# Optimization experiments

Measured on AMD Instinct MI355X. Metric: run time of the kernel, lower is better.

Reference implementation:

```python
import jax, jax.numpy as jnp
import numpy as np

H = 1024
EPS = 1e-5
MIX_SCALE = 0.1


def setup_inputs() -> dict:
    key = jax.random.key(0)
    ks = jax.random.split(key, 6)
    B, S = 8, 4096
    x = jax.random.normal(ks[0], (B, S, H), dtype=jnp.float32)
    # to_complex: Linear(H, 2H); store weight as [H, 2H] for x @ W
    W_to = jax.random.normal(ks[1], (H, 2 * H), dtype=jnp.float32) * (1.0 / np.sqrt(H))
    b_to = jax.random.normal(ks[2], (2 * H,), dtype=jnp.float32) * 0.01
    # from_complex: Linear(2H, H)
    W_from = jax.random.normal(ks[3], (2 * H, H), dtype=jnp.float32) * (1.0 / np.sqrt(2 * H))
    b_from = jax.random.normal(ks[4], (H,), dtype=jnp.float32) * 0.01
    phase_shifts = jnp.zeros((1, 1, H), dtype=jnp.float32)
    return {"x": x, "W_to": W_to, "b_to": b_to, "W_from": W_from,
            "b_from": b_from, "phase_shifts": phase_shifts}


def reference(x, W_to, b_to, W_from, b_from, phase_shifts):
    # x: [B,S,H]
    complex_repr = x @ W_to + b_to                      # [B,S,2H]
    real, imag = jnp.split(complex_repr, 2, axis=-1)    # each [B,S,H]
    magnitude = jnp.sqrt(real**2 + imag**2 + EPS)
    phase = jnp.arctan2(imag, real)                     # [B,S,H]
    # mean_j cos(phase_i - phase_j + shift)
    #   = cos(phase_i + shift) * mean_j cos(phase_j)
    #   + sin(phase_i + shift) * mean_j sin(phase_j)
    # (exact trig identity; replaces the [B,S,S,H] materialization)
    mean_cos = jnp.mean(jnp.cos(phase), axis=1, keepdims=True)  # [B,1,H]
    mean_sin = jnp.mean(jnp.sin(phase), axis=1, keepdims=True)  # [B,1,H]
    shifted = phase + phase_shifts                              # [B,S,H]
    mixed_phase = jnp.cos(shifted) * mean_cos + jnp.sin(shifted) * mean_sin
    new_phase = phase + mixed_phase * MIX_SCALE
    new_real = magnitude * jnp.cos(new_phase)
    new_imag = magnitude * jnp.sin(new_phase)
    new_complex = jnp.concatenate([new_real, new_imag], axis=-1)  # [B,S,2H]
    return new_complex @ W_from + b_from                          # [B,S,H]
```

## Files before the change

kernel.cpp:

```cpp
#include <hip/hip_runtime.h>
#include <hip/hip_bf16.h>
#include <math.h>

#define H 1024
#define N1 2048
#define BATCH 8
#define SEQ 4096
#define M_TOT (BATCH*SEQ)
#define EPS 1e-5f
#define MIX 0.1f

typedef __attribute__((ext_vector_type(8))) short bf16x8;
typedef __attribute__((ext_vector_type(4))) float f32x4;
typedef unsigned int uint_t;

static __device__ __forceinline__ float bf2f(unsigned short u) {
    return __uint_as_float(((unsigned)u) << 16);
}
static __device__ __forceinline__ unsigned short f2bf(float x) {
    __hip_bfloat16 h = __float2bfloat16(x);
    return *reinterpret_cast<unsigned short*>(&h);
}
static __device__ __forceinline__ void gload16(const void* g, void* l) {
    __builtin_amdgcn_global_load_lds(
        (const __attribute__((address_space(1))) unsigned int*)g,
        (__attribute__((address_space(3))) unsigned int*)l,
        16, 0, 0);
}
static __device__ __forceinline__ int perm2h(int c)  { return ((c & 1023) << 1) | (c >> 10); }

__global__ __launch_bounds__(256) void cvt_f32_bf16(
    const float* __restrict__ in, unsigned short* __restrict__ out, size_t n)
{
    size_t i = ((size_t)blockIdx.x * 256 + threadIdx.x) * 8;
    if (i >= n) return;
    float4 a = *(const float4*)(in + i);
    float4 b = *(const float4*)(in + i + 4);
    union { unsigned short u[8]; uint4 v; } p;
    p.u[0] = f2bf(a.x); p.u[1] = f2bf(a.y); p.u[2] = f2bf(a.z); p.u[3] = f2bf(a.w);
    p.u[4] = f2bf(b.x); p.u[5] = f2bf(b.y); p.u[6] = f2bf(b.z); p.u[7] = f2bf(b.w);
    *(uint4*)(out + i) = p.v;
}

__global__ __launch_bounds__(256) void transpose_wt(
    const float* __restrict__ in, unsigned short* __restrict__ out)
{
    __shared__ float tile[64][65];
    const int c0 = blockIdx.x * 64, r0 = blockIdx.y * 64;
    const int tc = threadIdx.x & 63, tr4 = (threadIdx.x >> 6) * 16;
    #pragma unroll
    for (int rr = 0; rr < 16; ++rr)
        tile[tr4 + rr][tc] = in[(size_t)(r0 + tr4 + rr) * N1 + c0 + tc];
    __syncthreads();
    #pragma unroll
    for (int rr = 0; rr < 16; ++rr)
        out[(size_t)perm2h(c0 + tr4 + rr) * H + r0 + tc] = f2bf(tile[tc][tr4 + rr]);
}

__global__ __launch_bounds__(256) void transpose_wf(
    const float* __restrict__ in, unsigned short* __restrict__ out)
{
    __shared__ float tile[64][65];
    const int n0 = blockIdx.x * 64, k0 = blockIdx.y * 64;
    const int tc = threadIdx.x & 63, tr4 = (threadIdx.x >> 6) * 16;
    #pragma unroll
    for (int rr = 0; rr < 16; ++rr) {
        const int k = k0 + tr4 + rr;
        tile[tr4 + rr][tc] = in[(size_t)((k >> 1) | ((k & 1) << 10)) * H + n0 + tc];
    }
    __syncthreads();
    #pragma unroll
    for (int rr = 0; rr < 16; ++rr)
        out[(size_t)(n0 + tr4 + rr) * N1 + k0 + tc] = f2bf(tile[tc][tr4 + rr]);
}

#define VM4 asm volatile("s_waitcnt vmcnt(4)" ::: "memory")
#define VM0 asm volatile("s_waitcnt vmcnt(0)" ::: "memory")

#define STG(X, BB, HH, CC, TT) \
    gload16(X##g + (size_t)((HH)*128 + (CC)*64) * KDIM + (TT)*64, \
            &X##s[BB][(HH)*8192 + (CC)*4096 + t*8])
#define STAGE_HT(X, BB, HH, TT) do { STG(X, BB, HH, 0, TT); STG(X, BB, HH, 1, TT); } while(0)

#define LDA(BB, MF, KS) (*(const bf16x8*)&As[BB][(wr*128 + (MF)*16 + fr)*64 + ((((KS)*4 + lg) ^ rsw))*8])
#define LDB(BB, NF, KS) (*(const bf16x8*)&Bs[BB][(wc*64  + (NF)*16 + fr)*64 + ((((KS)*4 + lg) ^ rsw))*8])

#define PHASE(BB, Q, STAGE_STMT, VM_STMT) do {                                  \
    if ((Q) == 0) {                                                             \
        _Pragma("unroll")                                                       \
        for (int nf = 0; nf < 4; ++nf) {                                        \
            bfr[nf][0] = LDB(BB, nf, 0);                                        \
            bfr[nf][1] = LDB(BB, nf, 1);                                        \
        }                                                                       \
    }                                                                           \
    afr[0][0] = LDA(BB, 2*(Q),   0); afr[0][1] = LDA(BB, 2*(Q),   1);           \
    afr[1][0] = LDA(BB, 2*(Q)+1, 0); afr[1][1] = LDA(BB, 2*(Q)+1, 1);           \
    STAGE_STMT;                                                                 \
    __builtin_amdgcn_s_barrier();                                               \
    asm volatile("s_waitcnt lgkmcnt(0)" ::: "memory");                          \
    __builtin_amdgcn_sched_barrier(0);                                          \
    __builtin_amdgcn_s_setprio(1);                                              \
    _Pragma("unroll")                                                           \
    for (int nf = 0; nf < 4; ++nf) {                                            \
        acc[2*(Q)][nf]   = __builtin_amdgcn_mfma_f32_16x16x32_bf16(afr[0][0], bfr[nf][0], acc[2*(Q)][nf],   0,0,0); \
        acc[2*(Q)][nf]   = __builtin_amdgcn_mfma_f32_16x16x32_bf16(afr[0][1], bfr[nf][1], acc[2*(Q)][nf],   0,0,0); \
        acc[2*(Q)+1][nf] = __builtin_amdgcn_mfma_f32_16x16x32_bf16(afr[1][0], bfr[nf][0], acc[2*(Q)+1][nf], 0,0,0); \
        acc[2*(Q)+1][nf] = __builtin_amdgcn_mfma_f32_16x16x32_bf16(afr[1][1], bfr[nf][1], acc[2*(Q)+1][nf], 0,0,0); \
    }                                                                           \
    __builtin_amdgcn_s_setprio(0);                                              \
    VM_STMT;                                                                    \
    __builtin_amdgcn_s_barrier();                                               \
} while (0)

template<int KDIM, bool G1>
__global__ __launch_bounds__(512, 2) void gemm8(
    const unsigned short* __restrict__ A,
    const unsigned short* __restrict__ Bt,
    const float* __restrict__ bias,
    void* __restrict__ Cout,
    float* __restrict__ sums)
{
    __shared__ __align__(16) unsigned short As[2][16384];
    __shared__ __align__(16) unsigned short Bs[2][16384];

    const int t    = threadIdx.x;
    const int lane = t & 63;
    const int wid  = t >> 6;
    const int wr   = wid >> 2;
    const int wc   = wid & 3;

    int m0, n0;
    if (G1) {
        const unsigned wg = ((blockIdx.x & 7) << 7) | (blockIdx.x >> 3);
        n0 = (wg & 7) * 256;
        m0 = (wg >> 3) * 256;
    } else {
        const unsigned wg = ((blockIdx.x & 7) << 6) | (blockIdx.x >> 3);
        n0 = (wg & 3) * 256;
        m0 = (wg >> 2) * 256;
    }

    const int srow = t >> 3;
    const int ssw  = ((srow >> 1) & 1) | (((srow >> 2) & 1) << 1);
    const int gk   = ((t & 7) ^ ssw) * 8;
    const unsigned short* Ag = A  + (size_t)(m0 + srow) * KDIM + gk;
    const unsigned short* Bg = Bt + (size_t)(n0 + srow) * KDIM + gk;

    const int fr  = lane & 15;
    const int lg  = lane >> 4;
    const int rsw = ((fr >> 1) & 1) | (((fr >> 2) & 1) << 1);

    f32x4 acc[8][4] = {};
    bf16x8 bfr[4][2];
    bf16x8 afr[2][2];

    constexpr int NITER = KDIM / 128;

    STAGE_HT(A, 0, 0, 0); STAGE_HT(A, 0, 1, 0);
    STAGE_HT(B, 0, 0, 0); STAGE_HT(B, 0, 1, 0);
    STAGE_HT(B, 1, 0, 1); STAGE_HT(B, 1, 1, 1);
    VM4;
    __builtin_amdgcn_s_barrier();

    for (int it = 0; it < NITER; ++it) {
        const int  T1   = 2 * it + 1;
        const int  T2   = 2 * it + 2;
        const int  T3   = 2 * it + 3;
        const bool more = (it + 1 < NITER);
        PHASE(0, 0, STAGE_HT(A, 1, 0, T1), );
        PHASE(0, 1, STAGE_HT(A, 1, 1, T1), );
        PHASE(0, 2, if (more) STAGE_HT(B, 0, 0, T2), );
        PHASE(0, 3, if (more) STAGE_HT(B, 0, 1, T2), if (more) { VM4; } else { VM0; });
        PHASE(1, 0, if (more) STAGE_HT(A, 0, 0, T2), );
        PHASE(1, 1, if (more) STAGE_HT(A, 0, 1, T2), );
        PHASE(1, 2, if (more) STAGE_HT(B, 1, 0, T3), );
        PHASE(1, 3, if (more) STAGE_HT(B, 1, 1, T3), if (more) { VM4; });
    }

    const int colbase = n0 + wc * 64;
    if (G1) {
        unsigned short* c1 = (unsigned short*)Cout;
        float lc[4] = {0, 0, 0, 0}, ls[4] = {0, 0, 0, 0};
        #pragma unroll
        for (int nf = 0; nf < 4; ++nf) {
            const int col = colbase + nf * 16 + fr;
            const float bb = bias[(col >> 1) | ((col & 1) << 10)];
            #pragma unroll
            for (int mf = 0; mf < 8; ++mf) {
                #pragma unroll
                for (int r = 0; r < 4; ++r) {
                    const float v = acc[mf][nf][r] + bb;
                    const size_t row = (size_t)(m0 + wr * 128 + mf * 16 + lg * 4 + r);
                    c1[row * N1 + col] = f2bf(v);
                    const float oth = __shfl_xor(v, 1);
                    const float re = (fr & 1) ? oth : v;
                    const float im = (fr & 1) ? v : oth;
                    const float rq = rsqrtf(fmaxf(re * re + im * im, 1e-30f));
                    lc[nf] += re * rq;
                    ls[nf] += im * rq;
                }
            }
        }
        #pragma unroll
        for (int nf = 0; nf < 4; ++nf) {
            lc[nf] += __shfl_xor(lc[nf], 16); lc[nf] += __shfl_xor(lc[nf], 32);
            ls[nf] += __shfl_xor(ls[nf], 16); ls[nf] += __shfl_xor(ls[nf], 32);
        }
        if (lane < 16 && !(lane & 1)) {
            const int b = m0 >> 12;
            #pragma unroll
            for (int nf = 0; nf < 4; ++nf) {
                const int hh = (colbase + nf * 16 + fr) >> 1;
                atomicAdd(&sums[(b * 2 + 0) * H + hh], lc[nf]);
                atomicAdd(&sums[(b * 2 + 1) * H + hh], ls[nf]);
            }
        }
    } else {
        float* o = (float*)Cout;
        #pragma unroll
        for (int nf = 0; nf < 4; ++nf) {
            const int col = colbase + nf * 16 + fr;
            const float bb = bias[col];
            #pragma unroll
            for (int mf = 0; mf < 8; ++mf) {
                #pragma unroll
                for (int r = 0; r < 4; ++r) {
                    const size_t row = (size_t)(m0 + wr * 128 + mf * 16 + lg * 4 + r);
                    o[row * H + col] = acc[mf][nf][r] + bb;
                }
            }
        }
    }
}

__global__ void finalize_pq(const float* __restrict__ sums, const float* __restrict__ ps,
                            float* __restrict__ P, float* __restrict__ Q)
{
    int i = blockIdx.x * 256 + threadIdx.x;
    int b = i >> 10, h = i & (H - 1);
    float mc = sums[(b * 2 + 0) * H + h] * (1.0f / SEQ);
    float ms = sums[(b * 2 + 1) * H + h] * (1.0f / SEQ);
    float cp = cosf(ps[h]), sp = sinf(ps[h]);
    P[i] = mc * cp + ms * sp;
    Q[i] = ms * cp - mc * sp;
}

__global__ __launch_bounds__(256) void phase_mix(
    unsigned short* __restrict__ c1, const float* __restrict__ P,
    const float* __restrict__ Q)
{
    const size_t total = (size_t)M_TOT * N1 / 8;
    for (size_t q = (size_t)blockIdx.x * 256 + threadIdx.x; q < total;
         q += (size_t)gridDim.x * 256) {
        const size_t m = q >> 8;
        const int off = ((int)q & 255) * 8;
        const int b = (int)(m >> 12);
        const int h0 = off >> 1;
        uint4* cu = (uint4*)c1;
        const size_t idx = ((size_t)m * N1 + off) >> 3;
        uint4 v = cu[idx];
        float4 Pv = *(const float4*)&P[b * H + h0];
        float4 Qv = *(const float4*)&Q[b * H + h0];
        const uint_t w[4] = { v.x, v.y, v.z, v.w };
        const float Pk[4] = { Pv.x, Pv.y, Pv.z, Pv.w };
        const float Qk[4] = { Qv.x, Qv.y, Qv.z, Qv.w };
        uint_t o[4];
        #pragma unroll
        for (int e = 0; e < 4; ++e) {
            float r  = bf2f(w[e] & 0xffff);
            float im = bf2f(w[e] >> 16);
            float tt = r * r + im * im;
            float minv = rsqrtf(fmaxf(tt, 1e-30f));
            float d = MIX * (r * Pk[e] + im * Qk[e]) * minv;
            float d2 = d * d;
            float cd = 1.0f - d2 * (0.5f - d2 * (1.0f / 24.0f));
            float sd = d * (1.0f - d2 * ((1.0f / 6.0f) - d2 * (1.0f / 120.0f)));
            float sc = sqrtf(tt + EPS) * minv;
            o[e] = (uint_t)f2bf(sc * (r * cd - im * sd))
                 | ((uint_t)f2bf(sc * (im * cd + r * sd)) << 16);
        }
        v.x = o[0]; v.y = o[1]; v.z = o[2]; v.w = o[3];
        cu[idx] = v;
    }
}

extern "C" void kernel_launch(void* const* d_in, const int* in_sizes, int n_in,
                              void* d_out, int out_size, void* d_ws, size_t ws_size,
                              hipStream_t stream) {
    const float* x  = (const float*)d_in[0];
    const float* Wt = (const float*)d_in[1];
    const float* bt = (const float*)d_in[2];
    const float* Wf = (const float*)d_in[3];
    const float* bf = (const float*)d_in[4];
    const float* ps = (const float*)d_in[5];
    float* out = (float*)d_out;

    const size_t c1_bytes   = (size_t)M_TOT * N1 * 2;
    const size_t wft_bytes  = (size_t)H * N1 * 2;
    const size_t sums_bytes = (size_t)BATCH * 2 * H * 4;
    const size_t pq_bytes   = (size_t)BATCH * H * 4;
    if (ws_size < c1_bytes + wft_bytes + sums_bytes + 2 * pq_bytes) return;

    unsigned short* c1  = (unsigned short*)d_ws;
    unsigned short* WfT = (unsigned short*)((char*)d_ws + c1_bytes);
    float* sums = (float*)((char*)d_ws + c1_bytes + wft_bytes);
    float* Pb   = (float*)((char*)d_ws + c1_bytes + wft_bytes + sums_bytes);
    float* Qb   = (float*)((char*)d_ws + c1_bytes + wft_bytes + sums_bytes + pq_bytes);

    unsigned short* xb  = (unsigned short*)d_out;
    unsigned short* WtT = (unsigned short*)d_out + (size_t)M_TOT * H;

    hipMemsetAsync(sums, 0, sums_bytes, stream);

    cvt_f32_bf16<<<dim3((unsigned)(((size_t)M_TOT * H / 8 + 255) / 256)), 256, 0, stream>>>(
        x, xb, (size_t)M_TOT * H);
    transpose_wt<<<dim3(N1 / 64, H / 64), 256, 0, stream>>>(Wt, WtT);
    transpose_wf<<<dim3(H / 64, N1 / 64), 256, 0, stream>>>(Wf, WfT);

    gemm8<H, true><<<dim3(1024), 512, 0, stream>>>(xb, WtT, bt, (void*)c1, sums);

    finalize_pq<<<dim3(BATCH * H / 256), 256, 0, stream>>>(sums, ps, Pb, Qb);
    phase_mix<<<dim3(4096), 256, 0, stream>>>(c1, Pb, Qb);

    gemm8<N1, false><<<dim3(512), 512, 0, stream>>>(c1, WfT, bf, (void*)out, nullptr);
}
```

Measured before the change: 397.0 us.

## Stage GEMM1 bf16 output through LDS for coalesced 16-byte stores; widen LDS swizzle

The first GEMM epilogue now adds the bias in place, computes the phase sums, then writes each 16x64 bf16 tile to a per-wave LDS scratch area (reusing the A tile buffer) and stores it to global memory as 16-byte vectors instead of scattered 2-byte stores. Separately, the LDS XOR swizzle now uses three row bits instead of two to reduce bank conflicts on the fragment loads. The epilogue gains extra LDS traffic, and reusing the A buffer assumes all waves have finished their main-loop reads before the scratch writes; no barrier guards this.

```diff
diff --git a/kernel.cpp b/kernel.cpp
--- a/kernel.cpp
+++ b/kernel.cpp
@@ -141,14 +141,14 @@
     }
 
     const int srow = t >> 3;
-    const int ssw  = ((srow >> 1) & 1) | (((srow >> 2) & 1) << 1);
+    const int ssw  = srow & 7;
     const int gk   = ((t & 7) ^ ssw) * 8;
     const unsigned short* Ag = A  + (size_t)(m0 + srow) * KDIM + gk;
     const unsigned short* Bg = Bt + (size_t)(n0 + srow) * KDIM + gk;
 
     const int fr  = lane & 15;
     const int lg  = lane >> 4;
-    const int rsw = ((fr >> 1) & 1) | (((fr >> 2) & 1) << 1);
+    const int rsw = fr & 7;
 
     f32x4 acc[8][4] = {};
     bf16x8 bfr[4][2];
@@ -180,18 +180,24 @@
     const int colbase = n0 + wc * 64;
     if (G1) {
         unsigned short* c1 = (unsigned short*)Cout;
-        float lc[4] = {0, 0, 0, 0}, ls[4] = {0, 0, 0, 0};
         #pragma unroll
         for (int nf = 0; nf < 4; ++nf) {
             const int col = colbase + nf * 16 + fr;
             const float bb = bias[(col >> 1) | ((col & 1) << 10)];
             #pragma unroll
-            for (int mf = 0; mf < 8; ++mf) {
+            for (int mf = 0; mf < 8; ++mf)
+                #pragma unroll
+                for (int r = 0; r < 4; ++r)
+                    acc[mf][nf][r] += bb;
+        }
+        float lc[4] = {0, 0, 0, 0}, ls[4] = {0, 0, 0, 0};
+        #pragma unroll
+        for (int nf = 0; nf < 4; ++nf)
+            #pragma unroll
+            for (int mf = 0; mf < 8; ++mf)
                 #pragma unroll
                 for (int r = 0; r < 4; ++r) {
-                    const float v = acc[mf][nf][r] + bb;
-                    const size_t row = (size_t)(m0 + wr * 128 + mf * 16 + lg * 4 + r);
-                    c1[row * N1 + col] = f2bf(v);
+                    const float v = acc[mf][nf][r];
                     const float oth = __shfl_xor(v, 1);
                     const float re = (fr & 1) ? oth : v;
                     const float im = (fr & 1) ? v : oth;
@@ -199,8 +205,6 @@
                     lc[nf] += re * rq;
                     ls[nf] += im * rq;
                 }
-            }
-        }
         #pragma unroll
         for (int nf = 0; nf < 4; ++nf) {
             lc[nf] += __shfl_xor(lc[nf], 16); lc[nf] += __shfl_xor(lc[nf], 32);
@@ -213,6 +217,23 @@
                 const int hh = (colbase + nf * 16 + fr) >> 1;
                 atomicAdd(&sums[(b * 2 + 0) * H + hh], lc[nf]);
                 atomicAdd(&sums[(b * 2 + 1) * H + hh], ls[nf]);
+            }
+        }
+        unsigned short* cst = &As[0][0] + wid * 2048;
+        const int row16 = lane >> 2;
+        #pragma unroll
+        for (int mf = 0; mf < 8; ++mf) {
+            #pragma unroll
+            for (int nf = 0; nf < 4; ++nf)
+                #pragma unroll
+                for (int r = 0; r < 4; ++r)
+                    cst[(lg * 4 + r) * 68 + nf * 16 + fr] = f2bf(acc[mf][nf][r]);
+            const size_t grow = (size_t)(m0 + wr * 128 + mf * 16 + row16);
+            #pragma unroll
+            for (int c = 0; c < 2; ++c) {
+                const int chunk = (lane & 3) + c * 4;
+                uint4 v = *(const uint4*)&cst[row16 * 68 + chunk * 8];
+                *(uint4*)&c1[grow * N1 + colbase + chunk * 8] = v;
             }
         }
     } else {
```

New measurement: 366.7 us. 7.6% less time.
